# Performance work log

Measured on AMD Instinct MI355X. Metric: run time of the kernel, lower is better.

## Reference

```python
import jax, jax.numpy as jnp
import numpy as np

N_NODES = 100000
N_EDGES = 1600000
IN_DIM = 128
OUT_DIM = 64
EDGE_DIM = 8


def setup_inputs() -> dict:
    key = jax.random.key(0)
    ks = jax.random.split(key, 7)
    h = jax.random.normal(ks[0], (N_NODES, IN_DIM), dtype=jnp.float32)
    edge_index = jax.random.randint(ks[1], (2, N_EDGES), 0, N_NODES, dtype=jnp.int64)
    edge_attr = jax.random.normal(ks[2], (N_EDGES, EDGE_DIM), dtype=jnp.float32)
    w_w = jax.random.normal(ks[3], (IN_DIM, OUT_DIM), dtype=jnp.float32) * (1.0 / np.sqrt(IN_DIM))
    w_b = jax.random.normal(ks[4], (OUT_DIM,), dtype=jnp.float32) * 0.01
    a_w = jax.random.normal(ks[5], (2 * OUT_DIM + EDGE_DIM, 1), dtype=jnp.float32) * 0.1
    a_b = jax.random.normal(ks[6], (1,), dtype=jnp.float32) * 0.01
    return {"h": h, "edge_index": edge_index, "edge_attr": edge_attr,
            "w_w": w_w, "w_b": w_b, "a_w": a_w, "a_b": a_b}


def reference(h, edge_index, edge_attr, w_w, w_b, a_w, a_b):
    n = h.shape[0]
    d = w_w.shape[1]
    wh = h @ w_w + w_b                              # [N, out_dim]
    row, col = edge_index[0], edge_index[1]
    # a([wh[row], wh[col], edge_attr]) == wh[row]@a1 + wh[col]@a2 + edge_attr@a3 + b
    a1, a2, a3 = a_w[:d], a_w[d:2 * d], a_w[2 * d:]
    s_row = wh @ a1                                 # [N, 1] per-node attention terms
    s_col = wh @ a2                                 # [N, 1]
    e = jax.nn.leaky_relu(s_row[row] + s_col[col] + edge_attr @ a3 + a_b)  # [E, 1]
    # segment softmax over edges grouped by destination `row`
    max_e = jax.ops.segment_max(e, row, num_segments=n)     # [N, 1]
    alpha = jnp.exp(e - max_e[row])                          # [E, 1]
    out = jax.ops.segment_sum(alpha * wh[col], row, num_segments=n)  # [N, out_dim]
    norm = jax.ops.segment_sum(alpha, row, num_segments=n)           # [N, 1]
    return out / (norm + 1e-8)
```

## Files before the change

### kernel.cpp

```cpp
#include <hip/hip_runtime.h>
#include <hip/hip_fp16.h>

#define IN_DIM 128
#define OUT_DIM 64
#define RPB 128
#define MAXB 800
#define EPB 4096
#define ENTL 2304
#define CAP 3584
#define NWH 320

typedef __attribute__((ext_vector_type(8))) _Float16 half8;
typedef __attribute__((ext_vector_type(4))) float f32x4;

__global__ __launch_bounds__(256) void k_zero(int* __restrict__ gcur) {
  for (int i = threadIdx.x; i < MAXB; i += 256) gcur[i] = 0;
}

__global__ __launch_bounds__(512) void k_whfill(
    const float* __restrict__ h, const float* __restrict__ w_w,
    const float* __restrict__ w_b, const float* __restrict__ a_w,
    const int* __restrict__ ei, const float* __restrict__ edge_attr,
    __half* __restrict__ wh, float* __restrict__ s_row,
    float* __restrict__ s_col, int* __restrict__ gcur,
    int2* __restrict__ entA, int n_nodes, int nedges, int nb, int nfill) {
  if ((int)blockIdx.x < nfill) {
    __shared__ int hist[MAXB];
    __shared__ int cbase[MAXB];
    __shared__ int curs[MAXB];
    for (int b = threadIdx.x; b < MAXB; b += 512) hist[b] = 0;
    const float aw0 = a_w[128], aw1 = a_w[129], aw2 = a_w[130], aw3 = a_w[131];
    const float aw4 = a_w[132], aw5 = a_w[133], aw6 = a_w[134], aw7 = a_w[135];
    __syncthreads();
    const int e0 = blockIdx.x * EPB;
    int row[8], col[8];
    float s[8];
#pragma unroll
    for (int k = 0; k < 8; ++k) {
      int e = e0 + k * 512 + threadIdx.x;
      if (e < nedges) {
        row[k] = ei[e];
        col[k] = ei[nedges + e];
      } else {
        row[k] = -1;
        col[k] = 0;
      }
    }
#pragma unroll
    for (int k = 0; k < 8; ++k) {
      int e = e0 + k * 512 + threadIdx.x;
      if (row[k] >= 0) {
        const float4* ea = (const float4*)(edge_attr + (size_t)e * 8);
        float4 u = ea[0], v = ea[1];
        float t = u.x * aw0 + u.y * aw1 + u.z * aw2 + u.w * aw3;
        t += v.x * aw4 + v.y * aw5 + v.z * aw6 + v.w * aw7;
        s[k] = t;
      } else {
        s[k] = 0.f;
      }
    }
#pragma unroll
    for (int k = 0; k < 8; ++k)
      if (row[k] >= 0) atomicAdd(&hist[row[k] >> 7], 1);
    __syncthreads();
    for (int b = threadIdx.x; b < nb; b += 512) {
      int c = hist[b];
      int cb = 0;
      if (c > 0) cb = b * CAP + atomicAdd(&gcur[b], (c + 7) & ~7);
      cbase[b] = cb;
      curs[b] = cb;
    }
    __syncthreads();
#pragma unroll
    for (int k = 0; k < 8; ++k) {
      if (row[k] >= 0) {
        int bb = row[k] >> 7;
        int pos = atomicAdd(&curs[bb], 1);
        entA[pos] = make_int2(((row[k] & 127) << 17) | col[k],
                              __float_as_int(s[k]));
      }
    }
    __syncthreads();
    for (int b = threadIdx.x; b < nb; b += 512) {
      int c = hist[b];
      if (c > 0) {
        int st = cbase[b] + c, end = cbase[b] + ((c + 7) & ~7);
        for (int k = st; k < end; ++k) entA[k] = make_int2(-1, 0);
      }
    }
  } else {
    __shared__ _Float16 wf[4 * 4 * 64 * 8];
    for (int idx = threadIdx.x; idx < IN_DIM * OUT_DIM; idx += 512) {
      int k = idx >> 6, c = idx & 63;
      int mt = c >> 4;
      int kt = k >> 5;
      int l = (((k >> 3) & 3) << 4) | (c & 15);
      int j = k & 7;
      wf[(((mt << 2) | kt) << 9) | (l << 3) | j] = (_Float16)w_w[idx];
    }
    __syncthreads();

    const int lane = threadIdx.x & 63;
    const int wv = threadIdx.x >> 6;

    half8 A[4][4];
#pragma unroll
    for (int mt = 0; mt < 4; ++mt)
#pragma unroll
      for (int kt = 0; kt < 4; ++kt)
        A[mt][kt] =
            *(const half8*)&wf[(((mt << 2) | kt) << 9) | (lane << 3)];

    const int cbase2 = (lane >> 4) << 2;
    f32x4 bq[4], a1q[4], a2q[4];
#pragma unroll
    for (int mt = 0; mt < 4; ++mt) {
      bq[mt] = *(const f32x4*)&w_b[mt * 16 + cbase2];
      a1q[mt] = *(const f32x4*)&a_w[mt * 16 + cbase2];
      a2q[mt] = *(const f32x4*)&a_w[OUT_DIM + mt * 16 + cbase2];
    }

    const int wb = blockIdx.x - nfill;
    const int ntiles = (n_nodes + 15) >> 4;
    const int tstride = NWH * 8;
    for (int t = wb * 8 + wv; t < ntiles; t += tstride) {
      const int n0 = t << 4;
      const int node = n0 + (lane & 15);
      const int nodec = node < n_nodes ? node : n_nodes - 1;
      const float4* hv =
          (const float4*)(h + (size_t)nodec * IN_DIM + ((lane >> 4) << 3));
      float4 p[8];
#pragma unroll
      for (int kt = 0; kt < 4; ++kt) {
        p[2 * kt] = hv[kt * 8];
        p[2 * kt + 1] = hv[kt * 8 + 1];
      }
      f32x4 C[4];
#pragma unroll
      for (int mt = 0; mt < 4; ++mt) C[mt] = (f32x4){0.f, 0.f, 0.f, 0.f};
#pragma unroll
      for (int kt = 0; kt < 4; ++kt) {
        const float4 u = p[2 * kt], v = p[2 * kt + 1];
        half8 B;
        B[0] = (_Float16)u.x; B[1] = (_Float16)u.y;
        B[2] = (_Float16)u.z; B[3] = (_Float16)u.w;
        B[4] = (_Float16)v.x; B[5] = (_Float16)v.y;
        B[6] = (_Float16)v.z; B[7] = (_Float16)v.w;
#pragma unroll
        for (int mt = 0; mt < 4; ++mt)
          C[mt] = __builtin_amdgcn_mfma_f32_16x16x32_f16(A[mt][kt], B, C[mt],
                                                         0, 0, 0);
      }
      float sr = 0.f, sc = 0.f;
      uint2 q[4];
#pragma unroll
      for (int mt = 0; mt < 4; ++mt) {
        f32x4 d = C[mt] + bq[mt];
        sr += d[0] * a1q[mt][0] + d[1] * a1q[mt][1] + d[2] * a1q[mt][2] +
              d[3] * a1q[mt][3];
        sc += d[0] * a2q[mt][0] + d[1] * a2q[mt][1] + d[2] * a2q[mt][2] +
              d[3] * a2q[mt][3];
        __half2 lo = __floats2half2_rn(d[0], d[1]);
        __half2 hi = __floats2half2_rn(d[2], d[3]);
        q[mt].x = *(unsigned int*)&lo;
        q[mt].y = *(unsigned int*)&hi;
      }
      if (node < n_nodes) {
        uint2* wrow = (uint2*)(wh + (size_t)node * OUT_DIM + cbase2);
        wrow[0] = q[0];
        wrow[4] = q[1];
        wrow[8] = q[2];
        wrow[12] = q[3];
      }
      sr += __shfl_xor(sr, 16, 64);
      sr += __shfl_xor(sr, 32, 64);
      sc += __shfl_xor(sc, 16, 64);
      sc += __shfl_xor(sc, 32, 64);
      if (lane < 16 && node < n_nodes) {
        s_row[node] = sr;
        s_col[node] = sc;
      }
    }
  }
}

__global__ __launch_bounds__(512) void k_sagg(
    const int2* __restrict__ entA, const int* __restrict__ gcur,
    const __half* __restrict__ wh,
    const float* __restrict__ s_row, const float* __restrict__ s_col,
    const float* __restrict__ a_b, float* __restrict__ out, int n_nodes) {
  __shared__ int2 entl[ENTL];
  __shared__ int hist[RPB], sd[RPB], starts[RPB], curs[RPB], degs[RPB];
  const int b = blockIdx.x;
  const int row0 = b << 7;
  const int t = threadIdx.x;
  if (t < RPB) hist[t] = 0;
  __syncthreads();
  const int c = gcur[b];
  const int base = b * CAP;
  int2 e[8];
#pragma unroll
  for (int k = 0; k < 8; ++k) {
    int i = t + k * 512;
    e[k] = (i < c) ? entA[base + i] : make_int2(-1, 0);
  }
#pragma unroll
  for (int k = 0; k < 8; ++k)
    if (e[k].x >= 0) atomicAdd(&hist[e[k].x >> 17], 1);
  for (int i = t + 4096; i < c; i += 512) {
    int2 p = entA[base + i];
    if (p.x >= 0) atomicAdd(&hist[p.x >> 17], 1);
  }
  __syncthreads();
  int hh = 0;
  if (t < RPB) { hh = hist[t]; sd[t] = hh; }
  __syncthreads();
  for (int off = 1; off < RPB; off <<= 1) {
    int x = (t >= off && t < RPB) ? sd[t - off] : 0;
    __syncthreads();
    if (t < RPB) sd[t] += x;
    __syncthreads();
  }
  if (t < RPB) {
    int excl = sd[t] - hh;
    starts[t] = excl;
    curs[t] = excl;
    degs[t] = hh;
  }
  __syncthreads();
#pragma unroll
  for (int k = 0; k < 8; ++k)
    if (e[k].x >= 0) {
      int p = atomicAdd(&curs[e[k].x >> 17], 1);
      if (p < ENTL) entl[p] = e[k];
    }
  for (int i = t + 4096; i < c; i += 512) {
    int2 p2 = entA[base + i];
    if (p2.x >= 0) {
      int p = atomicAdd(&curs[p2.x >> 17], 1);
      if (p < ENTL) entl[p] = p2;
    }
  }
  __syncthreads();
  const int wv = t >> 6;
  const int lane = t & 63;
  const int slot = lane >> 3, sub = lane & 7;
  const float ab = a_b[0];
  const uint4* whq = (const uint4*)wh;
  for (int j = 0; j < 16; ++j) {
    const int rl = wv * 16 + j;
    const int node = row0 + rl;
    if (node >= n_nodes) break;
    const int st = starts[rl];
    const int dg = degs[rl];
    const float sab = s_row[node] + ab;
    float acc[8] = {0.f, 0.f, 0.f, 0.f, 0.f, 0.f, 0.f, 0.f};
    float l = 0.f;
    for (int bas = 0; bas < dg; bas += 32) {
      const int i0 = bas + slot, i1 = i0 + 8, i2 = i0 + 16, i3 = i0 + 24;
      const bool g0 = i0 < dg, g1 = i1 < dg, g2 = i2 < dg, g3 = i3 < dg;
      int2 p0 = g0 ? entl[st + i0] : make_int2(0, 0);
      int2 p1 = g1 ? entl[st + i1] : make_int2(0, 0);
      int2 p2 = g2 ? entl[st + i2] : make_int2(0, 0);
      int2 p3 = g3 ? entl[st + i3] : make_int2(0, 0);
      const int col0 = p0.x & 0x1FFFF, col1 = p1.x & 0x1FFFF;
      const int col2 = p2.x & 0x1FFFF, col3 = p3.x & 0x1FFFF;
      uint4 q0 = make_uint4(0, 0, 0, 0), q1 = make_uint4(0, 0, 0, 0);
      uint4 q2 = make_uint4(0, 0, 0, 0), q3 = make_uint4(0, 0, 0, 0);
      float sc0 = 0.f, sc1 = 0.f, sc2 = 0.f, sc3 = 0.f;
      if (g0) { q0 = whq[(size_t)col0 * 8 + sub]; sc0 = s_col[col0]; }
      if (g1) { q1 = whq[(size_t)col1 * 8 + sub]; sc1 = s_col[col1]; }
      if (g2) { q2 = whq[(size_t)col2 * 8 + sub]; sc2 = s_col[col2]; }
      if (g3) { q3 = whq[(size_t)col3 * 8 + sub]; sc3 = s_col[col3]; }
      if (g0) {
        float s = sab + sc0 + __int_as_float(p0.y);
        float ev = (s > 0.f) ? s : 0.01f * s;
        float a = __expf(ev);
        float2 f0 = __half22float2(*(__half2*)&q0.x);
        float2 f1 = __half22float2(*(__half2*)&q0.y);
        float2 f2 = __half22float2(*(__half2*)&q0.z);
        float2 f3 = __half22float2(*(__half2*)&q0.w);
        acc[0] = fmaf(a, f0.x, acc[0]); acc[1] = fmaf(a, f0.y, acc[1]);
        acc[2] = fmaf(a, f1.x, acc[2]); acc[3] = fmaf(a, f1.y, acc[3]);
        acc[4] = fmaf(a, f2.x, acc[4]); acc[5] = fmaf(a, f2.y, acc[5]);
        acc[6] = fmaf(a, f3.x, acc[6]); acc[7] = fmaf(a, f3.y, acc[7]);
        if (sub == 0) l += a;
      }
      if (g1) {
        float s = sab + sc1 + __int_as_float(p1.y);
        float ev = (s > 0.f) ? s : 0.01f * s;
        float a = __expf(ev);
        float2 f0 = __half22float2(*(__half2*)&q1.x);
        float2 f1 = __half22float2(*(__half2*)&q1.y);
        float2 f2 = __half22float2(*(__half2*)&q1.z);
        float2 f3 = __half22float2(*(__half2*)&q1.w);
        acc[0] = fmaf(a, f0.x, acc[0]); acc[1] = fmaf(a, f0.y, acc[1]);
        acc[2] = fmaf(a, f1.x, acc[2]); acc[3] = fmaf(a, f1.y, acc[3]);
        acc[4] = fmaf(a, f2.x, acc[4]); acc[5] = fmaf(a, f2.y, acc[5]);
        acc[6] = fmaf(a, f3.x, acc[6]); acc[7] = fmaf(a, f3.y, acc[7]);
        if (sub == 0) l += a;
      }
      if (g2) {
        float s = sab + sc2 + __int_as_float(p2.y);
        float ev = (s > 0.f) ? s : 0.01f * s;
        float a = __expf(ev);
        float2 f0 = __half22float2(*(__half2*)&q2.x);
        float2 f1 = __half22float2(*(__half2*)&q2.y);
        float2 f2 = __half22float2(*(__half2*)&q2.z);
        float2 f3 = __half22float2(*(__half2*)&q2.w);
        acc[0] = fmaf(a, f0.x, acc[0]); acc[1] = fmaf(a, f0.y, acc[1]);
        acc[2] = fmaf(a, f1.x, acc[2]); acc[3] = fmaf(a, f1.y, acc[3]);
        acc[4] = fmaf(a, f2.x, acc[4]); acc[5] = fmaf(a, f2.y, acc[5]);
        acc[6] = fmaf(a, f3.x, acc[6]); acc[7] = fmaf(a, f3.y, acc[7]);
        if (sub == 0) l += a;
      }
      if (g3) {
        float s = sab + sc3 + __int_as_float(p3.y);
        float ev = (s > 0.f) ? s : 0.01f * s;
        float a = __expf(ev);
        float2 f0 = __half22float2(*(__half2*)&q3.x);
        float2 f1 = __half22float2(*(__half2*)&q3.y);
        float2 f2 = __half22float2(*(__half2*)&q3.z);
        float2 f3 = __half22float2(*(__half2*)&q3.w);
        acc[0] = fmaf(a, f0.x, acc[0]); acc[1] = fmaf(a, f0.y, acc[1]);
        acc[2] = fmaf(a, f1.x, acc[2]); acc[3] = fmaf(a, f1.y, acc[3]);
        acc[4] = fmaf(a, f2.x, acc[4]); acc[5] = fmaf(a, f2.y, acc[5]);
        acc[6] = fmaf(a, f3.x, acc[6]); acc[7] = fmaf(a, f3.y, acc[7]);
        if (sub == 0) l += a;
      }
    }
#pragma unroll
    for (int d = 0; d < 8; ++d) {
      acc[d] += __shfl_xor(acc[d], 8, 64);
      acc[d] += __shfl_xor(acc[d], 16, 64);
      acc[d] += __shfl_xor(acc[d], 32, 64);
    }
    l += __shfl_xor(l, 8, 64);
    l += __shfl_xor(l, 16, 64);
    l += __shfl_xor(l, 32, 64);
    float lt = __shfl(l, 0, 64);
    if (slot == 0) {
      float inv = 1.0f / (lt + 1e-8f);
      float4 o0 = make_float4(acc[0] * inv, acc[1] * inv, acc[2] * inv,
                              acc[3] * inv);
      float4 o1 = make_float4(acc[4] * inv, acc[5] * inv, acc[6] * inv,
                              acc[7] * inv);
      float4* orow = (float4*)out + (size_t)node * 16 + sub * 2;
      orow[0] = o0;
      orow[1] = o1;
    }
  }
}

extern "C" void kernel_launch(void* const* d_in, const int* in_sizes, int n_in,
                              void* d_out, int out_size, void* d_ws, size_t ws_size,
                              hipStream_t stream) {
  const float* h         = (const float*)d_in[0];
  const int*   ei        = (const int*)d_in[1];
  const float* edge_attr = (const float*)d_in[2];
  const float* w_w       = (const float*)d_in[3];
  const float* w_b       = (const float*)d_in[4];
  const float* a_w       = (const float*)d_in[5];
  const float* a_b       = (const float*)d_in[6];
  const int n_nodes = in_sizes[0] / IN_DIM;
  const int nedges  = in_sizes[1] / 2;
  const int nb   = (n_nodes + RPB - 1) / RPB;
  const int nebl = (nedges + EPB - 1) / EPB;

  __half* wh       = (__half*)d_ws;
  int2*  entA      = (int2*)(wh + (size_t)n_nodes * OUT_DIM);
  int*   gcur      = (int*)(entA + (size_t)nb * CAP);
  float* s_row     = (float*)(gcur + MAXB);
  float* s_col     = s_row + n_nodes;

  k_zero<<<1, 256, 0, stream>>>(gcur);
  k_whfill<<<nebl + NWH, 512, 0, stream>>>(h, w_w, w_b, a_w, ei, edge_attr,
                                           wh, s_row, s_col, gcur, entA,
                                           n_nodes, nedges, nb, nebl);
  k_sagg<<<nb, 512, 0, stream>>>(entA, gcur, wh, s_row, s_col, a_b,
                                 (float*)d_out, n_nodes);
}
```

Measured before the change: 220.8 us.

## Fuse zero, fill/transform and aggregation into one cooperative persistent kernel

Merges the three kernel launches into a single cooperative kernel that separates the phases with grid-wide syncs and handles work units through persistent block loops. Shared memory for the phases is overlaid in a union. This removes two launch gaps and inter-kernel drain bubbles. In exchange it adds grid.sync costs and caps the grid at occupancy×256, which may reduce parallelism in the aggregation phase (782 blocks) and make the shared-memory union size set occupancy.

```diff
diff --git a/kernel.cpp b/kernel.cpp
--- a/kernel.cpp
+++ b/kernel.cpp
@@ -1,5 +1,8 @@
 #include <hip/hip_runtime.h>
 #include <hip/hip_fp16.h>
+#include <hip/hip_cooperative_groups.h>
+
+namespace cg = cooperative_groups;
 
 #define IN_DIM 128
 #define OUT_DIM 64
@@ -13,341 +16,354 @@
 typedef __attribute__((ext_vector_type(8))) _Float16 half8;
 typedef __attribute__((ext_vector_type(4))) float f32x4;
 
-__global__ __launch_bounds__(256) void k_zero(int* __restrict__ gcur) {
-  for (int i = threadIdx.x; i < MAXB; i += 256) gcur[i] = 0;
-}
-
-__global__ __launch_bounds__(512) void k_whfill(
+struct SFill { int hist[MAXB]; int cb[MAXB]; int cur[MAXB]; };
+struct SWh   { _Float16 wf[4 * 4 * 64 * 8]; };
+struct SSagg {
+  int2 entl[ENTL];
+  int hist[RPB]; int sd[RPB]; int starts[RPB]; int curs[RPB]; int degs[RPB];
+};
+union SU { SFill f; SWh w; SSagg s; };
+
+__global__ __launch_bounds__(512) void k_all(
     const float* __restrict__ h, const float* __restrict__ w_w,
     const float* __restrict__ w_b, const float* __restrict__ a_w,
     const int* __restrict__ ei, const float* __restrict__ edge_attr,
     __half* __restrict__ wh, float* __restrict__ s_row,
     float* __restrict__ s_col, int* __restrict__ gcur,
-    int2* __restrict__ entA, int n_nodes, int nedges, int nb, int nfill) {
-  if ((int)blockIdx.x < nfill) {
-    __shared__ int hist[MAXB];
-    __shared__ int cbase[MAXB];
-    __shared__ int curs[MAXB];
-    for (int b = threadIdx.x; b < MAXB; b += 512) hist[b] = 0;
-    const float aw0 = a_w[128], aw1 = a_w[129], aw2 = a_w[130], aw3 = a_w[131];
-    const float aw4 = a_w[132], aw5 = a_w[133], aw6 = a_w[134], aw7 = a_w[135];
-    __syncthreads();
-    const int e0 = blockIdx.x * EPB;
-    int row[8], col[8];
-    float s[8];
-#pragma unroll
-    for (int k = 0; k < 8; ++k) {
-      int e = e0 + k * 512 + threadIdx.x;
-      if (e < nedges) {
-        row[k] = ei[e];
-        col[k] = ei[nedges + e];
-      } else {
-        row[k] = -1;
-        col[k] = 0;
-      }
-    }
-#pragma unroll
-    for (int k = 0; k < 8; ++k) {
-      int e = e0 + k * 512 + threadIdx.x;
-      if (row[k] >= 0) {
-        const float4* ea = (const float4*)(edge_attr + (size_t)e * 8);
-        float4 u = ea[0], v = ea[1];
-        float t = u.x * aw0 + u.y * aw1 + u.z * aw2 + u.w * aw3;
-        t += v.x * aw4 + v.y * aw5 + v.z * aw6 + v.w * aw7;
-        s[k] = t;
-      } else {
-        s[k] = 0.f;
-      }
-    }
-#pragma unroll
-    for (int k = 0; k < 8; ++k)
-      if (row[k] >= 0) atomicAdd(&hist[row[k] >> 7], 1);
-    __syncthreads();
-    for (int b = threadIdx.x; b < nb; b += 512) {
-      int c = hist[b];
-      int cb = 0;
-      if (c > 0) cb = b * CAP + atomicAdd(&gcur[b], (c + 7) & ~7);
-      cbase[b] = cb;
-      curs[b] = cb;
-    }
-    __syncthreads();
-#pragma unroll
-    for (int k = 0; k < 8; ++k) {
-      if (row[k] >= 0) {
-        int bb = row[k] >> 7;
-        int pos = atomicAdd(&curs[bb], 1);
-        entA[pos] = make_int2(((row[k] & 127) << 17) | col[k],
-                              __float_as_int(s[k]));
-      }
-    }
-    __syncthreads();
-    for (int b = threadIdx.x; b < nb; b += 512) {
-      int c = hist[b];
-      if (c > 0) {
-        int st = cbase[b] + c, end = cbase[b] + ((c + 7) & ~7);
-        for (int k = st; k < end; ++k) entA[k] = make_int2(-1, 0);
-      }
-    }
-  } else {
-    __shared__ _Float16 wf[4 * 4 * 64 * 8];
-    for (int idx = threadIdx.x; idx < IN_DIM * OUT_DIM; idx += 512) {
-      int k = idx >> 6, c = idx & 63;
-      int mt = c >> 4;
-      int kt = k >> 5;
-      int l = (((k >> 3) & 3) << 4) | (c & 15);
-      int j = k & 7;
-      wf[(((mt << 2) | kt) << 9) | (l << 3) | j] = (_Float16)w_w[idx];
-    }
-    __syncthreads();
-
-    const int lane = threadIdx.x & 63;
-    const int wv = threadIdx.x >> 6;
-
-    half8 A[4][4];
-#pragma unroll
-    for (int mt = 0; mt < 4; ++mt)
-#pragma unroll
-      for (int kt = 0; kt < 4; ++kt)
-        A[mt][kt] =
-            *(const half8*)&wf[(((mt << 2) | kt) << 9) | (lane << 3)];
-
-    const int cbase2 = (lane >> 4) << 2;
-    f32x4 bq[4], a1q[4], a2q[4];
-#pragma unroll
-    for (int mt = 0; mt < 4; ++mt) {
-      bq[mt] = *(const f32x4*)&w_b[mt * 16 + cbase2];
-      a1q[mt] = *(const f32x4*)&a_w[mt * 16 + cbase2];
-      a2q[mt] = *(const f32x4*)&a_w[OUT_DIM + mt * 16 + cbase2];
-    }
-
-    const int wb = blockIdx.x - nfill;
-    const int ntiles = (n_nodes + 15) >> 4;
-    const int tstride = NWH * 8;
-    for (int t = wb * 8 + wv; t < ntiles; t += tstride) {
-      const int n0 = t << 4;
-      const int node = n0 + (lane & 15);
-      const int nodec = node < n_nodes ? node : n_nodes - 1;
-      const float4* hv =
-          (const float4*)(h + (size_t)nodec * IN_DIM + ((lane >> 4) << 3));
-      float4 p[8];
-#pragma unroll
-      for (int kt = 0; kt < 4; ++kt) {
-        p[2 * kt] = hv[kt * 8];
-        p[2 * kt + 1] = hv[kt * 8 + 1];
-      }
-      f32x4 C[4];
-#pragma unroll
-      for (int mt = 0; mt < 4; ++mt) C[mt] = (f32x4){0.f, 0.f, 0.f, 0.f};
-#pragma unroll
-      for (int kt = 0; kt < 4; ++kt) {
-        const float4 u = p[2 * kt], v = p[2 * kt + 1];
-        half8 B;
-        B[0] = (_Float16)u.x; B[1] = (_Float16)u.y;
-        B[2] = (_Float16)u.z; B[3] = (_Float16)u.w;
-        B[4] = (_Float16)v.x; B[5] = (_Float16)v.y;
-        B[6] = (_Float16)v.z; B[7] = (_Float16)v.w;
-#pragma unroll
-        for (int mt = 0; mt < 4; ++mt)
-          C[mt] = __builtin_amdgcn_mfma_f32_16x16x32_f16(A[mt][kt], B, C[mt],
-                                                         0, 0, 0);
-      }
-      float sr = 0.f, sc = 0.f;
-      uint2 q[4];
+    int2* __restrict__ entA, const float* __restrict__ a_b,
+    float* __restrict__ out, int n_nodes, int nedges, int nb, int nfill) {
+  __shared__ SU sm;
+  cg::grid_group grid = cg::this_grid();
+
+  for (int i = blockIdx.x * 512 + threadIdx.x; i < MAXB;
+       i += gridDim.x * 512)
+    gcur[i] = 0;
+  __threadfence();
+  grid.sync();
+
+  const int nunits = nfill + NWH;
+  for (int u = blockIdx.x; u < nunits; u += gridDim.x) {
+    __syncthreads();
+    if (u < nfill) {
+      for (int b = threadIdx.x; b < MAXB; b += 512) sm.f.hist[b] = 0;
+      const float aw0 = a_w[128], aw1 = a_w[129], aw2 = a_w[130],
+                  aw3 = a_w[131];
+      const float aw4 = a_w[132], aw5 = a_w[133], aw6 = a_w[134],
+                  aw7 = a_w[135];
+      __syncthreads();
+      const int e0 = u * EPB;
+      int row[8], col[8];
+      float s[8];
+#pragma unroll
+      for (int k = 0; k < 8; ++k) {
+        int e = e0 + k * 512 + threadIdx.x;
+        if (e < nedges) {
+          row[k] = ei[e];
+          col[k] = ei[nedges + e];
+        } else {
+          row[k] = -1;
+          col[k] = 0;
+        }
+      }
+#pragma unroll
+      for (int k = 0; k < 8; ++k) {
+        int e = e0 + k * 512 + threadIdx.x;
+        if (row[k] >= 0) {
+          const float4* ea = (const float4*)(edge_attr + (size_t)e * 8);
+          float4 uu = ea[0], vv = ea[1];
+          float t = uu.x * aw0 + uu.y * aw1 + uu.z * aw2 + uu.w * aw3;
+          t += vv.x * aw4 + vv.y * aw5 + vv.z * aw6 + vv.w * aw7;
+          s[k] = t;
+        } else {
+          s[k] = 0.f;
+        }
+      }
+#pragma unroll
+      for (int k = 0; k < 8; ++k)
+        if (row[k] >= 0) atomicAdd(&sm.f.hist[row[k] >> 7], 1);
+      __syncthreads();
+      for (int b = threadIdx.x; b < nb; b += 512) {
+        int c = sm.f.hist[b];
+        int cb = 0;
+        if (c > 0) cb = b * CAP + atomicAdd(&gcur[b], (c + 7) & ~7);
+        sm.f.cb[b] = cb;
+        sm.f.cur[b] = cb;
+      }
+      __syncthreads();
+#pragma unroll
+      for (int k = 0; k < 8; ++k) {
+        if (row[k] >= 0) {
+          int bb = row[k] >> 7;
+          int pos = atomicAdd(&sm.f.cur[bb], 1);
+          entA[pos] = make_int2(((row[k] & 127) << 17) | col[k],
+                                __float_as_int(s[k]));
+        }
+      }
+      __syncthreads();
+      for (int b = threadIdx.x; b < nb; b += 512) {
+        int c = sm.f.hist[b];
+        if (c > 0) {
+          int st = sm.f.cb[b] + c, end = sm.f.cb[b] + ((c + 7) & ~7);
+          for (int k = st; k < end; ++k) entA[k] = make_int2(-1, 0);
+        }
+      }
+    } else {
+      for (int idx = threadIdx.x; idx < IN_DIM * OUT_DIM; idx += 512) {
+        int k = idx >> 6, c = idx & 63;
+        int mt = c >> 4;
+        int kt = k >> 5;
+        int l = (((k >> 3) & 3) << 4) | (c & 15);
+        int j = k & 7;
+        sm.w.wf[(((mt << 2) | kt) << 9) | (l << 3) | j] =
+            (_Float16)w_w[idx];
+      }
+      __syncthreads();
+
+      const int lane = threadIdx.x & 63;
+      const int wv = threadIdx.x >> 6;
+
+      half8 A[4][4];
+#pragma unroll
+      for (int mt = 0; mt < 4; ++mt)
+#pragma unroll
+        for (int kt = 0; kt < 4; ++kt)
+          A[mt][kt] =
+              *(const half8*)&sm.w.wf[(((mt << 2) | kt) << 9) | (lane << 3)];
+
+      const int cbase2 = (lane >> 4) << 2;
+      f32x4 bq[4], a1q[4], a2q[4];
 #pragma unroll
       for (int mt = 0; mt < 4; ++mt) {
-        f32x4 d = C[mt] + bq[mt];
-        sr += d[0] * a1q[mt][0] + d[1] * a1q[mt][1] + d[2] * a1q[mt][2] +
-              d[3] * a1q[mt][3];
-        sc += d[0] * a2q[mt][0] + d[1] * a2q[mt][1] + d[2] * a2q[mt][2] +
-              d[3] * a2q[mt][3];
-        __half2 lo = __floats2half2_rn(d[0], d[1]);
-        __half2 hi = __floats2half2_rn(d[2], d[3]);
-        q[mt].x = *(unsigned int*)&lo;
-        q[mt].y = *(unsigned int*)&hi;
-      }
-      if (node < n_nodes) {
-        uint2* wrow = (uint2*)(wh + (size_t)node * OUT_DIM + cbase2);
-        wrow[0] = q[0];
-        wrow[4] = q[1];
-        wrow[8] = q[2];
-        wrow[12] = q[3];
-      }
-      sr += __shfl_xor(sr, 16, 64);
-      sr += __shfl_xor(sr, 32, 64);
-      sc += __shfl_xor(sc, 16, 64);
-      sc += __shfl_xor(sc, 32, 64);
-      if (lane < 16 && node < n_nodes) {
-        s_row[node] = sr;
-        s_col[node] = sc;
+        bq[mt] = *(const f32x4*)&w_b[mt * 16 + cbase2];
+        a1q[mt] = *(const f32x4*)&a_w[mt * 16 + cbase2];
+        a2q[mt] = *(const f32x4*)&a_w[OUT_DIM + mt * 16 + cbase2];
+      }
+
+      const int wb = u - nfill;
+      const int ntiles = (n_nodes + 15) >> 4;
+      const int tstride = NWH * 8;
+      for (int t = wb * 8 + wv; t < ntiles; t += tstride) {
+        const int n0 = t << 4;
+        const int node = n0 + (lane & 15);
+        const int nodec = node < n_nodes ? node : n_nodes - 1;
+        const float4* hv =
+            (const float4*)(h + (size_t)nodec * IN_DIM + ((lane >> 4) << 3));
+        float4 p[8];
+#pragma unroll
+        for (int kt = 0; kt < 4; ++kt) {
+          p[2 * kt] = hv[kt * 8];
+          p[2 * kt + 1] = hv[kt * 8 + 1];
+        }
+        f32x4 C[4];
+#pragma unroll
+        for (int mt = 0; mt < 4; ++mt) C[mt] = (f32x4){0.f, 0.f, 0.f, 0.f};
+#pragma unroll
+        for (int kt = 0; kt < 4; ++kt) {
+          const float4 uu = p[2 * kt], vv = p[2 * kt + 1];
+          half8 B;
+          B[0] = (_Float16)uu.x; B[1] = (_Float16)uu.y;
+          B[2] = (_Float16)uu.z; B[3] = (_Float16)uu.w;
+          B[4] = (_Float16)vv.x; B[5] = (_Float16)vv.y;
+          B[6] = (_Float16)vv.z; B[7] = (_Float16)vv.w;
+#pragma unroll
+          for (int mt = 0; mt < 4; ++mt)
+            C[mt] = __builtin_amdgcn_mfma_f32_16x16x32_f16(A[mt][kt], B,
+                                                           C[mt], 0, 0, 0);
+        }
+        float sr = 0.f, sc = 0.f;
+        uint2 q[4];
+#pragma unroll
+        for (int mt = 0; mt < 4; ++mt) {
+          f32x4 d = C[mt] + bq[mt];
+          sr += d[0] * a1q[mt][0] + d[1] * a1q[mt][1] + d[2] * a1q[mt][2] +
+                d[3] * a1q[mt][3];
+          sc += d[0] * a2q[mt][0] + d[1] * a2q[mt][1] + d[2] * a2q[mt][2] +
+                d[3] * a2q[mt][3];
+          __half2 lo = __floats2half2_rn(d[0], d[1]);
+          __half2 hi = __floats2half2_rn(d[2], d[3]);
+          q[mt].x = *(unsigned int*)&lo;
+          q[mt].y = *(unsigned int*)&hi;
+        }
+        if (node < n_nodes) {
+          uint2* wrow = (uint2*)(wh + (size_t)node * OUT_DIM + cbase2);
+          wrow[0] = q[0];
+          wrow[4] = q[1];
+          wrow[8] = q[2];
+          wrow[12] = q[3];
+        }
+        sr += __shfl_xor(sr, 16, 64);
+        sr += __shfl_xor(sr, 32, 64);
+        sc += __shfl_xor(sc, 16, 64);
+        sc += __shfl_xor(sc, 32, 64);
+        if (lane < 16 && node < n_nodes) {
+          s_row[node] = sr;
+          s_col[node] = sc;
+        }
       }
     }
   }
-}
-
-__global__ __launch_bounds__(512) void k_sagg(
-    const int2* __restrict__ entA, const int* __restrict__ gcur,
-    const __half* __restrict__ wh,
-    const float* __restrict__ s_row, const float* __restrict__ s_col,
-    const float* __restrict__ a_b, float* __restrict__ out, int n_nodes) {
-  __shared__ int2 entl[ENTL];
-  __shared__ int hist[RPB], sd[RPB], starts[RPB], curs[RPB], degs[RPB];
-  const int b = blockIdx.x;
-  const int row0 = b << 7;
-  const int t = threadIdx.x;
-  if (t < RPB) hist[t] = 0;
-  __syncthreads();
-  const int c = gcur[b];
-  const int base = b * CAP;
-  int2 e[8];
-#pragma unroll
-  for (int k = 0; k < 8; ++k) {
-    int i = t + k * 512;
-    e[k] = (i < c) ? entA[base + i] : make_int2(-1, 0);
-  }
-#pragma unroll
-  for (int k = 0; k < 8; ++k)
-    if (e[k].x >= 0) atomicAdd(&hist[e[k].x >> 17], 1);
-  for (int i = t + 4096; i < c; i += 512) {
-    int2 p = entA[base + i];
-    if (p.x >= 0) atomicAdd(&hist[p.x >> 17], 1);
-  }
-  __syncthreads();
-  int hh = 0;
-  if (t < RPB) { hh = hist[t]; sd[t] = hh; }
-  __syncthreads();
-  for (int off = 1; off < RPB; off <<= 1) {
-    int x = (t >= off && t < RPB) ? sd[t - off] : 0;
-    __syncthreads();
-    if (t < RPB) sd[t] += x;
-    __syncthreads();
-  }
-  if (t < RPB) {
-    int excl = sd[t] - hh;
-    starts[t] = excl;
-    curs[t] = excl;
-    degs[t] = hh;
-  }
-  __syncthreads();
-#pragma unroll
-  for (int k = 0; k < 8; ++k)
-    if (e[k].x >= 0) {
-      int p = atomicAdd(&curs[e[k].x >> 17], 1);
-      if (p < ENTL) entl[p] = e[k];
-    }
-  for (int i = t + 4096; i < c; i += 512) {
-    int2 p2 = entA[base + i];
-    if (p2.x >= 0) {
-      int p = atomicAdd(&curs[p2.x >> 17], 1);
-      if (p < ENTL) entl[p] = p2;
-    }
-  }
-  __syncthreads();
-  const int wv = t >> 6;
-  const int lane = t & 63;
+  __threadfence();
+  grid.sync();
+
+  const int lane = threadIdx.x & 63;
+  const int wv = threadIdx.x >> 6;
   const int slot = lane >> 3, sub = lane & 7;
   const float ab = a_b[0];
   const uint4* whq = (const uint4*)wh;
-  for (int j = 0; j < 16; ++j) {
-    const int rl = wv * 16 + j;
-    const int node = row0 + rl;
-    if (node >= n_nodes) break;
-    const int st = starts[rl];
-    const int dg = degs[rl];
-    const float sab = s_row[node] + ab;
-    float acc[8] = {0.f, 0.f, 0.f, 0.f, 0.f, 0.f, 0.f, 0.f};
-    float l = 0.f;
-    for (int bas = 0; bas < dg; bas += 32) {
-      const int i0 = bas + slot, i1 = i0 + 8, i2 = i0 + 16, i3 = i0 + 24;
-      const bool g0 = i0 < dg, g1 = i1 < dg, g2 = i2 < dg, g3 = i3 < dg;
-      int2 p0 = g0 ? entl[st + i0] : make_int2(0, 0);
-      int2 p1 = g1 ? entl[st + i1] : make_int2(0, 0);
-      int2 p2 = g2 ? entl[st + i2] : make_int2(0, 0);
-      int2 p3 = g3 ? entl[st + i3] : make_int2(0, 0);
-      const int col0 = p0.x & 0x1FFFF, col1 = p1.x & 0x1FFFF;
-      const int col2 = p2.x & 0x1FFFF, col3 = p3.x & 0x1FFFF;
-      uint4 q0 = make_uint4(0, 0, 0, 0), q1 = make_uint4(0, 0, 0, 0);
-      uint4 q2 = make_uint4(0, 0, 0, 0), q3 = make_uint4(0, 0, 0, 0);
-      float sc0 = 0.f, sc1 = 0.f, sc2 = 0.f, sc3 = 0.f;
-      if (g0) { q0 = whq[(size_t)col0 * 8 + sub]; sc0 = s_col[col0]; }
-      if (g1) { q1 = whq[(size_t)col1 * 8 + sub]; sc1 = s_col[col1]; }
-      if (g2) { q2 = whq[(size_t)col2 * 8 + sub]; sc2 = s_col[col2]; }
-      if (g3) { q3 = whq[(size_t)col3 * 8 + sub]; sc3 = s_col[col3]; }
-      if (g0) {
-        float s = sab + sc0 + __int_as_float(p0.y);
-        float ev = (s > 0.f) ? s : 0.01f * s;
-        float a = __expf(ev);
-        float2 f0 = __half22float2(*(__half2*)&q0.x);
-        float2 f1 = __half22float2(*(__half2*)&q0.y);
-        float2 f2 = __half22float2(*(__half2*)&q0.z);
-        float2 f3 = __half22float2(*(__half2*)&q0.w);
-        acc[0] = fmaf(a, f0.x, acc[0]); acc[1] = fmaf(a, f0.y, acc[1]);
-        acc[2] = fmaf(a, f1.x, acc[2]); acc[3] = fmaf(a, f1.y, acc[3]);
-        acc[4] = fmaf(a, f2.x, acc[4]); acc[5] = fmaf(a, f2.y, acc[5]);
-        acc[6] = fmaf(a, f3.x, acc[6]); acc[7] = fmaf(a, f3.y, acc[7]);
-        if (sub == 0) l += a;
-      }
-      if (g1) {
-        float s = sab + sc1 + __int_as_float(p1.y);
-        float ev = (s > 0.f) ? s : 0.01f * s;
-        float a = __expf(ev);
-        float2 f0 = __half22float2(*(__half2*)&q1.x);
-        float2 f1 = __half22float2(*(__half2*)&q1.y);
-        float2 f2 = __half22float2(*(__half2*)&q1.z);
-        float2 f3 = __half22float2(*(__half2*)&q1.w);
-        acc[0] = fmaf(a, f0.x, acc[0]); acc[1] = fmaf(a, f0.y, acc[1]);
-        acc[2] = fmaf(a, f1.x, acc[2]); acc[3] = fmaf(a, f1.y, acc[3]);
-        acc[4] = fmaf(a, f2.x, acc[4]); acc[5] = fmaf(a, f2.y, acc[5]);
-        acc[6] = fmaf(a, f3.x, acc[6]); acc[7] = fmaf(a, f3.y, acc[7]);
-        if (sub == 0) l += a;
-      }
-      if (g2) {
-        float s = sab + sc2 + __int_as_float(p2.y);
-        float ev = (s > 0.f) ? s : 0.01f * s;
-        float a = __expf(ev);
-        float2 f0 = __half22float2(*(__half2*)&q2.x);
-        float2 f1 = __half22float2(*(__half2*)&q2.y);
-        float2 f2 = __half22float2(*(__half2*)&q2.z);
-        float2 f3 = __half22float2(*(__half2*)&q2.w);
-        acc[0] = fmaf(a, f0.x, acc[0]); acc[1] = fmaf(a, f0.y, acc[1]);
-        acc[2] = fmaf(a, f1.x, acc[2]); acc[3] = fmaf(a, f1.y, acc[3]);
-        acc[4] = fmaf(a, f2.x, acc[4]); acc[5] = fmaf(a, f2.y, acc[5]);
-        acc[6] = fmaf(a, f3.x, acc[6]); acc[7] = fmaf(a, f3.y, acc[7]);
-        if (sub == 0) l += a;
-      }
-      if (g3) {
-        float s = sab + sc3 + __int_as_float(p3.y);
-        float ev = (s > 0.f) ? s : 0.01f * s;
-        float a = __expf(ev);
-        float2 f0 = __half22float2(*(__half2*)&q3.x);
-        float2 f1 = __half22float2(*(__half2*)&q3.y);
-        float2 f2 = __half22float2(*(__half2*)&q3.z);
-        float2 f3 = __half22float2(*(__half2*)&q3.w);
-        acc[0] = fmaf(a, f0.x, acc[0]); acc[1] = fmaf(a, f0.y, acc[1]);
-        acc[2] = fmaf(a, f1.x, acc[2]); acc[3] = fmaf(a, f1.y, acc[3]);
-        acc[4] = fmaf(a, f2.x, acc[4]); acc[5] = fmaf(a, f2.y, acc[5]);
-        acc[6] = fmaf(a, f3.x, acc[6]); acc[7] = fmaf(a, f3.y, acc[7]);
-        if (sub == 0) l += a;
-      }
-    }
-#pragma unroll
-    for (int d = 0; d < 8; ++d) {
-      acc[d] += __shfl_xor(acc[d], 8, 64);
-      acc[d] += __shfl_xor(acc[d], 16, 64);
-      acc[d] += __shfl_xor(acc[d], 32, 64);
-    }
-    l += __shfl_xor(l, 8, 64);
-    l += __shfl_xor(l, 16, 64);
-    l += __shfl_xor(l, 32, 64);
-    float lt = __shfl(l, 0, 64);
-    if (slot == 0) {
-      float inv = 1.0f / (lt + 1e-8f);
-      float4 o0 = make_float4(acc[0] * inv, acc[1] * inv, acc[2] * inv,
-                              acc[3] * inv);
-      float4 o1 = make_float4(acc[4] * inv, acc[5] * inv, acc[6] * inv,
-                              acc[7] * inv);
-      float4* orow = (float4*)out + (size_t)node * 16 + sub * 2;
-      orow[0] = o0;
-      orow[1] = o1;
+  for (int b = blockIdx.x; b < nb; b += gridDim.x) {
+    __syncthreads();
+    const int row0 = b << 7;
+    const int t = threadIdx.x;
+    if (t < RPB) sm.s.hist[t] = 0;
+    __syncthreads();
+    const int c = gcur[b];
+    const int base = b * CAP;
+    int2 e[8];
+#pragma unroll
+    for (int k = 0; k < 8; ++k) {
+      int i = t + k * 512;
+      e[k] = (i < c) ? entA[base + i] : make_int2(-1, 0);
+    }
+#pragma unroll
+    for (int k = 0; k < 8; ++k)
+      if (e[k].x >= 0) atomicAdd(&sm.s.hist[e[k].x >> 17], 1);
+    for (int i = t + 4096; i < c; i += 512) {
+      int2 p = entA[base + i];
+      if (p.x >= 0) atomicAdd(&sm.s.hist[p.x >> 17], 1);
+    }
+    __syncthreads();
+    int hh = 0;
+    if (t < RPB) { hh = sm.s.hist[t]; sm.s.sd[t] = hh; }
+    __syncthreads();
+    for (int off = 1; off < RPB; off <<= 1) {
+      int x = (t >= off && t < RPB) ? sm.s.sd[t - off] : 0;
+      __syncthreads();
+      if (t < RPB) sm.s.sd[t] += x;
+      __syncthreads();
+    }
+    if (t < RPB) {
+      int excl = sm.s.sd[t] - hh;
+      sm.s.starts[t] = excl;
+      sm.s.curs[t] = excl;
+      sm.s.degs[t] = hh;
+    }
+    __syncthreads();
+#pragma unroll
+    for (int k = 0; k < 8; ++k)
+      if (e[k].x >= 0) {
+        int p = atomicAdd(&sm.s.curs[e[k].x >> 17], 1);
+        if (p < ENTL) sm.s.entl[p] = e[k];
+      }
+    for (int i = t + 4096; i < c; i += 512) {
+      int2 p2 = entA[base + i];
+      if (p2.x >= 0) {
+        int p = atomicAdd(&sm.s.curs[p2.x >> 17], 1);
+        if (p < ENTL) sm.s.entl[p] = p2;
+      }
+    }
+    __syncthreads();
+    for (int j = 0; j < 16; ++j) {
+      const int rl = wv * 16 + j;
+      const int node = row0 + rl;
+      if (node >= n_nodes) break;
+      const int st = sm.s.starts[rl];
+      const int dg = sm.s.degs[rl];
+      const float sab = s_row[node] + ab;
+      float acc[8] = {0.f, 0.f, 0.f, 0.f, 0.f, 0.f, 0.f, 0.f};
+      float l = 0.f;
+      for (int bas = 0; bas < dg; bas += 32) {
+        const int i0 = bas + slot, i1 = i0 + 8, i2 = i0 + 16, i3 = i0 + 24;
+        const bool g0 = i0 < dg, g1 = i1 < dg, g2 = i2 < dg, g3 = i3 < dg;
+        int2 p0 = g0 ? sm.s.entl[st + i0] : make_int2(0, 0);
+        int2 p1 = g1 ? sm.s.entl[st + i1] : make_int2(0, 0);
+        int2 p2 = g2 ? sm.s.entl[st + i2] : make_int2(0, 0);
+        int2 p3 = g3 ? sm.s.entl[st + i3] : make_int2(0, 0);
+        const int col0 = p0.x & 0x1FFFF, col1 = p1.x & 0x1FFFF;
+        const int col2 = p2.x & 0x1FFFF, col3 = p3.x & 0x1FFFF;
+        uint4 q0 = make_uint4(0, 0, 0, 0), q1 = make_uint4(0, 0, 0, 0);
+        uint4 q2 = make_uint4(0, 0, 0, 0), q3 = make_uint4(0, 0, 0, 0);
+        float sc0 = 0.f, sc1 = 0.f, sc2 = 0.f, sc3 = 0.f;
+        if (g0) { q0 = whq[(size_t)col0 * 8 + sub]; sc0 = s_col[col0]; }
+        if (g1) { q1 = whq[(size_t)col1 * 8 + sub]; sc1 = s_col[col1]; }
+        if (g2) { q2 = whq[(size_t)col2 * 8 + sub]; sc2 = s_col[col2]; }
+        if (g3) { q3 = whq[(size_t)col3 * 8 + sub]; sc3 = s_col[col3]; }
+        if (g0) {
+          float s = sab + sc0 + __int_as_float(p0.y);
+          float ev = (s > 0.f) ? s : 0.01f * s;
+          float a = __expf(ev);
+          float2 f0 = __half22float2(*(__half2*)&q0.x);
+          float2 f1 = __half22float2(*(__half2*)&q0.y);
+          float2 f2 = __half22float2(*(__half2*)&q0.z);
+          float2 f3 = __half22float2(*(__half2*)&q0.w);
+          acc[0] = fmaf(a, f0.x, acc[0]); acc[1] = fmaf(a, f0.y, acc[1]);
+          acc[2] = fmaf(a, f1.x, acc[2]); acc[3] = fmaf(a, f1.y, acc[3]);
+          acc[4] = fmaf(a, f2.x, acc[4]); acc[5] = fmaf(a, f2.y, acc[5]);
+          acc[6] = fmaf(a, f3.x, acc[6]); acc[7] = fmaf(a, f3.y, acc[7]);
+          if (sub == 0) l += a;
+        }
+        if (g1) {
+          float s = sab + sc1 + __int_as_float(p1.y);
+          float ev = (s > 0.f) ? s : 0.01f * s;
+          float a = __expf(ev);
+          float2 f0 = __half22float2(*(__half2*)&q1.x);
+          float2 f1 = __half22float2(*(__half2*)&q1.y);
+          float2 f2 = __half22float2(*(__half2*)&q1.z);
+          float2 f3 = __half22float2(*(__half2*)&q1.w);
+          acc[0] = fmaf(a, f0.x, acc[0]); acc[1] = fmaf(a, f0.y, acc[1]);
+          acc[2] = fmaf(a, f1.x, acc[2]); acc[3] = fmaf(a, f1.y, acc[3]);
+          acc[4] = fmaf(a, f2.x, acc[4]); acc[5] = fmaf(a, f2.y, acc[5]);
+          acc[6] = fmaf(a, f3.x, acc[6]); acc[7] = fmaf(a, f3.y, acc[7]);
+          if (sub == 0) l += a;
+        }
+        if (g2) {
+          float s = sab + sc2 + __int_as_float(p2.y);
+          float ev = (s > 0.f) ? s : 0.01f * s;
+          float a = __expf(ev);
+          float2 f0 = __half22float2(*(__half2*)&q2.x);
+          float2 f1 = __half22float2(*(__half2*)&q2.y);
+          float2 f2 = __half22float2(*(__half2*)&q2.z);
+          float2 f3 = __half22float2(*(__half2*)&q2.w);
+          acc[0] = fmaf(a, f0.x, acc[0]); acc[1] = fmaf(a, f0.y, acc[1]);
+          acc[2] = fmaf(a, f1.x, acc[2]); acc[3] = fmaf(a, f1.y, acc[3]);
+          acc[4] = fmaf(a, f2.x, acc[4]); acc[5] = fmaf(a, f2.y, acc[5]);
+          acc[6] = fmaf(a, f3.x, acc[6]); acc[7] = fmaf(a, f3.y, acc[7]);
+          if (sub == 0) l += a;
+        }
+        if (g3) {
+          float s = sab + sc3 + __int_as_float(p3.y);
+          float ev = (s > 0.f) ? s : 0.01f * s;
+          float a = __expf(ev);
+          float2 f0 = __half22float2(*(__half2*)&q3.x);
+          float2 f1 = __half22float2(*(__half2*)&q3.y);
+          float2 f2 = __half22float2(*(__half2*)&q3.z);
+          float2 f3 = __half22float2(*(__half2*)&q3.w);
+          acc[0] = fmaf(a, f0.x, acc[0]); acc[1] = fmaf(a, f0.y, acc[1]);
+          acc[2] = fmaf(a, f1.x, acc[2]); acc[3] = fmaf(a, f1.y, acc[3]);
+          acc[4] = fmaf(a, f2.x, acc[4]); acc[5] = fmaf(a, f2.y, acc[5]);
+          acc[6] = fmaf(a, f3.x, acc[6]); acc[7] = fmaf(a, f3.y, acc[7]);
+          if (sub == 0) l += a;
+        }
+      }
+#pragma unroll
+      for (int d = 0; d < 8; ++d) {
+        acc[d] += __shfl_xor(acc[d], 8, 64);
+        acc[d] += __shfl_xor(acc[d], 16, 64);
+        acc[d] += __shfl_xor(acc[d], 32, 64);
+      }
+      l += __shfl_xor(l, 8, 64);
+      l += __shfl_xor(l, 16, 64);
+      l += __shfl_xor(l, 32, 64);
+      float lt = __shfl(l, 0, 64);
+      if (slot == 0) {
+        float inv = 1.0f / (lt + 1e-8f);
+        float4 o0 = make_float4(acc[0] * inv, acc[1] * inv, acc[2] * inv,
+                                acc[3] * inv);
+        float4 o1 = make_float4(acc[4] * inv, acc[5] * inv, acc[6] * inv,
+                                acc[7] * inv);
+        float4* orow = (float4*)out + (size_t)node * 16 + sub * 2;
+        orow[0] = o0;
+        orow[1] = o1;
+      }
     }
   }
 }
@@ -362,21 +378,28 @@
   const float* w_b       = (const float*)d_in[4];
   const float* a_w       = (const float*)d_in[5];
   const float* a_b       = (const float*)d_in[6];
-  const int n_nodes = in_sizes[0] / IN_DIM;
-  const int nedges  = in_sizes[1] / 2;
-  const int nb   = (n_nodes + RPB - 1) / RPB;
-  const int nebl = (nedges + EPB - 1) / EPB;
+  int n_nodes = in_sizes[0] / IN_DIM;
+  int nedges  = in_sizes[1] / 2;
+  int nb   = (n_nodes + RPB - 1) / RPB;
+  int nfill = (nedges + EPB - 1) / EPB;
 
   __half* wh       = (__half*)d_ws;
   int2*  entA      = (int2*)(wh + (size_t)n_nodes * OUT_DIM);
   int*   gcur      = (int*)(entA + (size_t)nb * CAP);
   float* s_row     = (float*)(gcur + MAXB);
   float* s_col     = s_row + n_nodes;
-
-  k_zero<<<1, 256, 0, stream>>>(gcur);
-  k_whfill<<<nebl + NWH, 512, 0, stream>>>(h, w_w, w_b, a_w, ei, edge_attr,
-                                           wh, s_row, s_col, gcur, entA,
-                                           n_nodes, nedges, nb, nebl);
-  k_sagg<<<nb, 512, 0, stream>>>(entA, gcur, wh, s_row, s_col, a_b,
-                                 (float*)d_out, n_nodes);
+  float* outp      = (float*)d_out;
+
+  static int maxb = -1;
+  if (maxb < 0) {
+    hipOccupancyMaxActiveBlocksPerMultiprocessor(&maxb, k_all, 512, 0);
+    if (maxb < 1) maxb = 1;
+  }
+  int grid = maxb * 256;
+  if (grid > 1024) grid = 1024;
+
+  void* args[] = {&h, &w_w, &w_b, &a_w, &ei, &edge_attr, &wh, &s_row,
+                  &s_col, &gcur, &entA, &a_b, &outp, &n_nodes, &nedges,
+                  &nb, &nfill};
+  hipLaunchCooperativeKernel(k_all, dim3(grid), dim3(512), args, 0, stream);
 }
```

Result: slower. 456.8 us (+106.9%).
